# Performance work log

Measured on AMD Instinct MI355X. Metric: run time of the kernel, lower is better.

Reference implementation:

```python
import jax, jax.numpy as jnp
import numpy as np

H = 1024   # hidden size
E = 8      # num experts
B, S = 4, 2048


def setup_inputs() -> dict:
    key = jax.random.key(0)
    k1, k2, k3, k4 = jax.random.split(key, 4)
    x = jax.random.normal(k1, (B, S, H), dtype=jnp.float32)
    wg = jax.random.normal(k2, (H, E), dtype=jnp.float32) * 0.02      # gate weight
    W = jax.random.normal(k3, (E, H, H), dtype=jnp.float32) * 0.02    # expert Linear weights (out, in) per expert
    b = jax.random.normal(k4, (E, H), dtype=jnp.float32) * 0.02       # expert Linear biases
    return {"x": x, "wg": wg, "W": W, "b": b}


def reference(x, wg, W, b):
    Bb, Ss, Hh = x.shape
    Ee = wg.shape[1]
    T = Bb * Ss
    C = T // Ee  # capacity (capacity_factor = 1.0, top-1)

    xt = x.reshape(T, Hh)
    logits = xt @ wg                                   # [T, E]
    probs = jax.nn.softmax(logits, axis=-1)            # [T, E]
    idx = jnp.argmax(probs, axis=-1)                   # [T] top-1 expert
    mask = jax.nn.one_hot(idx, Ee, dtype=xt.dtype)     # [T, E]

    # position of each token within its expert's queue (0-based)
    locations = jnp.cumsum(mask, axis=0) - mask        # [T, E]
    # drop tokens over capacity
    mask = mask * (locations < C).astype(xt.dtype)
    gate = jnp.sum(probs * mask, axis=-1)              # [T] gate prob (0 if dropped)
    loc_s = jnp.sum(locations * mask, axis=-1).astype(jnp.int32)  # [T]
    loc_oh = jax.nn.one_hot(loc_s, C, dtype=xt.dtype)  # [T, C]

    dispatch = mask[:, :, None] * loc_oh[:, None, :]   # [T, E, C]
    combine = gate[:, None, None] * dispatch           # [T, E, C]

    # dispatch tokens -> per-expert buffers [E, C, H]
    exp_in = jnp.einsum('tec,th->ech', dispatch, xt)
    # per-expert Linear: y = x @ W_e^T + b_e
    exp_out = jnp.einsum('ech,efh->ecf', exp_in, W) + b[:, None, :]
    # combine back to tokens, scaled by gate prob
    out = jnp.einsum('tec,ecf->tf', combine, exp_out)  # [T, H]
    return out.reshape(Bb, Ss, Hh)
```

## Files before the change

kernel.cpp:

```cpp
#include <hip/hip_runtime.h>

#define H 1024
#define E 8
#define T 8192
#define CAP 1024

typedef __bf16 bf16x8 __attribute__((ext_vector_type(8)));
typedef float  f32x4  __attribute__((ext_vector_type(4)));
typedef unsigned short u16;

__device__ __forceinline__ u16 f2bf(float f) {
    union { float f; unsigned u; } v; v.f = f;
    unsigned r = v.u + 0x7FFFu + ((v.u >> 16) & 1u);
    return (u16)(r >> 16);
}

typedef __attribute__((address_space(1))) const void* gas_t;
typedef __attribute__((address_space(3))) void* las_t;
__device__ __forceinline__ void gld16(const void* g, void* l) {
    __builtin_amdgcn_global_load_lds((gas_t)g, (las_t)l, 16, 0, 0);
}

#define GATE_BLOCKS 512
#define CVT_BLOCKS  1536

__global__ __launch_bounds__(256) void gatecvt_kernel(
    const float* __restrict__ x, const float* __restrict__ wg,
    const float* __restrict__ W,
    int* __restrict__ eid, float* __restrict__ gate,
    u16* __restrict__ xbf, u16* __restrict__ Wbf) {
    const int tid = threadIdx.x;

    if (blockIdx.x >= GATE_BLOCKS) {
        int i = (blockIdx.x - GATE_BLOCKS) * 256 + tid;
        const int n4 = E * H * H / 4;
        const int stride = CVT_BLOCKS * 256;
        for (; i < n4; i += stride) {
            float4 v = ((const float4*)W)[i];
            ushort4 o;
            o.x = f2bf(v.x); o.y = f2bf(v.y); o.z = f2bf(v.z); o.w = f2bf(v.w);
            ((ushort4*)Wbf)[i] = o;
        }
        return;
    }

    const int wv = tid >> 6, lane = tid & 63;
    const int tbase = blockIdx.x * 16 + wv * 4;
    const int h00 = lane * 4;

    float a[4][8];
    #pragma unroll
    for (int j = 0; j < 4; ++j)
        #pragma unroll
        for (int e = 0; e < 8; ++e) a[j][e] = 0.f;

    #pragma unroll
    for (int q = 0; q < 4; ++q) {
        const int h0 = q * 256 + h00;
        float4 xv[4];
        #pragma unroll
        for (int j = 0; j < 4; ++j)
            xv[j] = *(const float4*)(x + (size_t)(tbase + j) * H + h0);
        #pragma unroll
        for (int j = 0; j < 4; ++j) {
            ushort4 o;
            o.x = f2bf(xv[j].x); o.y = f2bf(xv[j].y);
            o.z = f2bf(xv[j].z); o.w = f2bf(xv[j].w);
            *(ushort4*)(xbf + (size_t)(tbase + j) * H + h0) = o;
        }
        float wr[4][8];
        #pragma unroll
        for (int r = 0; r < 4; ++r) {
            const float4* p = (const float4*)(wg + (size_t)(h0 + r) * E);
            float4 lo = p[0], hi = p[1];
            wr[r][0] = lo.x; wr[r][1] = lo.y; wr[r][2] = lo.z; wr[r][3] = lo.w;
            wr[r][4] = hi.x; wr[r][5] = hi.y; wr[r][6] = hi.z; wr[r][7] = hi.w;
        }
        #pragma unroll
        for (int e = 0; e < 8; ++e)
            #pragma unroll
            for (int j = 0; j < 4; ++j)
                a[j][e] += xv[j].x * wr[0][e] + xv[j].y * wr[1][e]
                         + xv[j].z * wr[2][e] + xv[j].w * wr[3][e];
    }

    const bool b0 = lane & 1, b1 = lane & 2, b2 = lane & 4;
    const int elane = ((lane & 1) << 2) | (lane & 2) | ((lane >> 2) & 1);

    #pragma unroll
    for (int j = 0; j < 4; ++j) {
        float* A = a[j];
        #pragma unroll
        for (int k = 0; k < 4; ++k) {
            float t = b0 ? A[k] : A[k + 4];
            t = __shfl_xor(t, 1);
            A[k] = (b0 ? A[k + 4] : A[k]) + t;
        }
        #pragma unroll
        for (int k = 0; k < 2; ++k) {
            float t = b1 ? A[k] : A[k + 2];
            t = __shfl_xor(t, 2);
            A[k] = (b1 ? A[k + 2] : A[k]) + t;
        }
        {
            float t = b2 ? A[0] : A[1];
            t = __shfl_xor(t, 4);
            A[0] = (b2 ? A[1] : A[0]) + t;
        }
        float v = A[0];
        v += __shfl_xor(v, 8); v += __shfl_xor(v, 16); v += __shfl_xor(v, 32);
        float m = v; int mi = elane;
        #pragma unroll
        for (int off = 1; off <= 4; off <<= 1) {
            float om = __shfl_xor(m, off);
            int   oi = __shfl_xor(mi, off);
            if (om > m || (om == m && oi < mi)) { m = om; mi = oi; }
        }
        float s = expf(v - m);
        s += __shfl_xor(s, 1); s += __shfl_xor(s, 2); s += __shfl_xor(s, 4);
        if (lane == 0) {
            eid[tbase + j]  = mi;
            gate[tbase + j] = 1.0f / s;
        }
    }
}

#define SCAN_T 1024
#define STPT 8
__global__ __launch_bounds__(1024) void scan_kernel(
    const int* __restrict__ eid, float* __restrict__ gate,
    int* __restrict__ perm) {
    __shared__ int cnt[SCAN_T][E];
    __shared__ int part[E][32];
    const int tid = threadIdx.x;

    for (int i = tid; i < E * CAP; i += SCAN_T) perm[i] = -1;

    const int t0 = tid * STPT;
    int ei[STPT];
    #pragma unroll
    for (int i = 0; i < STPT; ++i) ei[i] = eid[t0 + i];

    int c[E];
    #pragma unroll
    for (int e = 0; e < E; ++e) c[e] = 0;
    #pragma unroll
    for (int i = 0; i < STPT; ++i)
        #pragma unroll
        for (int e = 0; e < E; ++e) c[e] += (ei[i] == e);
    #pragma unroll
    for (int e = 0; e < E; ++e) cnt[tid][e] = c[e];
    __syncthreads();

    if (tid < 256) {
        const int e = tid >> 5, g = tid & 31;
        int s = 0;
        for (int i = g * 32; i < g * 32 + 32; ++i) s += cnt[i][e];
        part[e][g] = s;
    }
    __syncthreads();
    if (tid < E) {
        int run = 0;
        #pragma unroll
        for (int g = 0; g < 32; ++g) { int v = part[tid][g]; part[tid][g] = run; run += v; }
    }
    __syncthreads();
    if (tid < 256) {
        const int e = tid >> 5, g = tid & 31;
        int run = part[e][g];
        for (int i = g * 32; i < g * 32 + 32; ++i) { int v = cnt[i][e]; cnt[i][e] = run; run += v; }
    }
    __syncthreads();

    #pragma unroll
    for (int e = 0; e < E; ++e) c[e] = cnt[tid][e];
    #pragma unroll
    for (int i = 0; i < STPT; ++i) {
        const int t = t0 + i, e0 = ei[i];
        int pos = 0;
        #pragma unroll
        for (int k = 0; k < E; ++k) if (e0 == k) pos = c[k]++;
        if (pos < CAP) perm[e0 * CAP + pos] = t;
        else gate[t] = 0.f;
    }
}

__global__ __launch_bounds__(512, 2) void moe_gemm_bf(
    const u16* __restrict__ xbf, const u16* __restrict__ Wbf,
    const float* __restrict__ bias, const int* __restrict__ perm,
    const float* __restrict__ gate, float* __restrict__ out) {
    __shared__ __align__(16) u16 As[3][256 * 64];
    __shared__ __align__(16) u16 Bs[3][128 * 64];
    __shared__ int   perm_s[256];
    __shared__ float gate_s[256];

    const int tid = threadIdx.x;
    const int bid = blockIdx.x;

    if (bid < 64) {
        const int t = bid * 128 + (tid >> 2);
        if (gate[t] == 0.f) {
            const int part = tid & 3;
            float4 z = make_float4(0.f, 0.f, 0.f, 0.f);
            float4* o = (float4*)(out + (size_t)t * H + part * 256);
            #pragma unroll
            for (int i = 0; i < 64; ++i) o[i] = z;
        }
        return;
    }

    const int idx = bid - 64;
    const int e  = idx & 7;
    const int mb = (idx >> 3) & 3;
    const int fb = idx >> 5;

    if (tid < 256) {
        const int t = perm[e * CAP + mb * 256 + tid];
        perm_s[tid] = t;
        gate_s[tid] = (t >= 0) ? gate[t] : 0.f;
    }
    __syncthreads();

    const int lane = tid & 63;
    const int wv = tid >> 6;
    const int wm2 = wv >> 1;
    const int wn2 = wv & 1;
    const int l16 = lane & 15, quad = lane >> 4;

    const int rl  = lane >> 3;
    const int cch = lane & 7;
    const int gch = cch ^ rl;

    const u16* ga[4];
    #pragma unroll
    for (int q = 0; q < 4; ++q) {
        const int r = q * 64 + wv * 8 + rl;
        const int tA = perm_s[r];
        const int tok = tA >= 0 ? tA : 0;
        ga[q] = xbf + (size_t)tok * H + gch * 8;
    }
    const u16* gb[2];
    #pragma unroll
    for (int q = 0; q < 2; ++q) {
        const int r = fb * 128 + q * 64 + wv * 8 + rl;
        gb[q] = Wbf + (size_t)e * H * H + (size_t)r * H + gch * 8;
    }

#define STAGE(BUF, TT)                                                        \
    {                                                                         \
        _Pragma("unroll")                                                     \
        for (int q = 0; q < 4; ++q)                                           \
            gld16(ga[q] + (TT) * 64, &As[BUF][(q * 64 + wv * 8) * 64 + lane * 8]); \
        _Pragma("unroll")                                                     \
        for (int q = 0; q < 2; ++q)                                           \
            gld16(gb[q] + (TT) * 64, &Bs[BUF][(q * 64 + wv * 8) * 64 + lane * 8]); \
    }

    f32x4 acc[4][4] = {};

    STAGE(0, 0)
    STAGE(1, 1)
    asm volatile("s_waitcnt vmcnt(6)" ::: "memory");
    __builtin_amdgcn_sched_barrier(0);
    __builtin_amdgcn_s_barrier();
    __builtin_amdgcn_sched_barrier(0);

    int cur = 0;
    #pragma unroll 1
    for (int t = 0; t < 16; ++t) {
        int nx2 = cur + 2; if (nx2 >= 3) nx2 -= 3;
        if (t < 14) STAGE(nx2, t + 2)

        const u16* cA = As[cur];
        const u16* cB = Bs[cur];
        #pragma unroll
        for (int kh = 0; kh < 2; ++kh) {
            bf16x8 af[4], bf[4];
            const int cc = (kh * 4 + quad) ^ (l16 & 7);
            #pragma unroll
            for (int mi = 0; mi < 4; ++mi)
                af[mi] = *(const bf16x8*)&cA[(wm2 * 64 + mi * 16 + l16) * 64 + cc * 8];
            #pragma unroll
            for (int ni = 0; ni < 4; ++ni)
                bf[ni] = *(const bf16x8*)&cB[(wn2 * 64 + ni * 16 + l16) * 64 + cc * 8];
            #pragma unroll
            for (int mi = 0; mi < 4; ++mi)
                #pragma unroll
                for (int ni = 0; ni < 4; ++ni)
                    acc[mi][ni] = __builtin_amdgcn_mfma_f32_16x16x32_bf16(
                        af[mi], bf[ni], acc[mi][ni], 0, 0, 0);
        }
        if (t == 15) break;

        __builtin_amdgcn_sched_barrier(0);
        if (t < 14) asm volatile("s_waitcnt vmcnt(6)" ::: "memory");
        else        asm volatile("s_waitcnt vmcnt(0)" ::: "memory");
        __builtin_amdgcn_sched_barrier(0);
        __builtin_amdgcn_s_barrier();
        __builtin_amdgcn_sched_barrier(0);
        cur = (cur == 2) ? 0 : cur + 1;
    }
#undef STAGE

    float bv[4];
    #pragma unroll
    for (int ni = 0; ni < 4; ++ni)
        bv[ni] = bias[e * H + fb * 128 + wn2 * 64 + ni * 16 + l16];

    #pragma unroll
    for (int mi = 0; mi < 4; ++mi) {
        #pragma unroll
        for (int r = 0; r < 4; ++r) {
            const int rowl = wm2 * 64 + mi * 16 + quad * 4 + r;
            const int t = perm_s[rowl];
            if (t < 0) continue;
            const float g = gate_s[rowl];
            float* orow = out + (size_t)t * H + fb * 128 + wn2 * 64;
            #pragma unroll
            for (int ni = 0; ni < 4; ++ni)
                orow[ni * 16 + l16] = g * (acc[mi][ni][r] + bv[ni]);
        }
    }
}

extern "C" void kernel_launch(void* const* d_in, const int* in_sizes, int n_in,
                              void* d_out, int out_size, void* d_ws, size_t ws_size,
                              hipStream_t stream) {
    const float* x    = (const float*)d_in[0];
    const float* wg   = (const float*)d_in[1];
    const float* W    = (const float*)d_in[2];
    const float* bias = (const float*)d_in[3];
    float* out = (float*)d_out;

    int*   eid  = (int*)d_ws;
    float* gate = (float*)((char*)d_ws + (size_t)T * 4);
    int*   perm = (int*)((char*)d_ws + (size_t)T * 8);
    u16*   xbf  = (u16*)((char*)d_ws + (size_t)T * 12);
    u16*   Wbf  = xbf + (size_t)T * H;

    gatecvt_kernel<<<GATE_BLOCKS + CVT_BLOCKS, 256, 0, stream>>>(
        x, wg, W, eid, gate, xbf, Wbf);
    scan_kernel<<<1, SCAN_T, 0, stream>>>(eid, gate, perm);
    moe_gemm_bf<<<64 + 256, 512, 0, stream>>>(xbf, Wbf, bias, perm, gate, out);
}
```

Before: 158.9 us.

## Shrink GEMM tiles to 128x128 with double buffering for more blocks and occupancy

The expert GEMM tile drops from 256x128 to 128x128 with two LDS buffers instead of three, so the grid doubles to 512 compute blocks and launch bounds allow 4 blocks per CU. Each wave now computes a 64x32 sub-tile, and MFMA sections get raised wave priority via s_setprio. The aim is better CU fill on 256 CUs and more waves to hide latency. In exchange each tile reuses less data, global traffic for W rises, and the shallower prefetch waits on vmcnt(0) every step.

```diff
diff --git a/kernel.cpp b/kernel.cpp
--- a/kernel.cpp
+++ b/kernel.cpp
@@ -185,14 +185,14 @@
     }
 }
 
-__global__ __launch_bounds__(512, 2) void moe_gemm_bf(
+__global__ __launch_bounds__(512, 4) void moe_gemm_bf(
     const u16* __restrict__ xbf, const u16* __restrict__ Wbf,
     const float* __restrict__ bias, const int* __restrict__ perm,
     const float* __restrict__ gate, float* __restrict__ out) {
-    __shared__ __align__(16) u16 As[3][256 * 64];
-    __shared__ __align__(16) u16 Bs[3][128 * 64];
-    __shared__ int   perm_s[256];
-    __shared__ float gate_s[256];
+    __shared__ __align__(16) u16 As[2][128 * 64];
+    __shared__ __align__(16) u16 Bs[2][128 * 64];
+    __shared__ int   perm_s[128];
+    __shared__ float gate_s[128];
 
     const int tid = threadIdx.x;
     const int bid = blockIdx.x;
@@ -211,11 +211,11 @@
 
     const int idx = bid - 64;
     const int e  = idx & 7;
-    const int mb = (idx >> 3) & 3;
-    const int fb = idx >> 5;
-
-    if (tid < 256) {
-        const int t = perm[e * CAP + mb * 256 + tid];
+    const int mb = (idx >> 3) & 7;
+    const int fb = idx >> 6;
+
+    if (tid < 128) {
+        const int t = perm[e * CAP + mb * 128 + tid];
         perm_s[tid] = t;
         gate_s[tid] = (t >= 0) ? gate[t] : 0.f;
     }
@@ -223,101 +223,96 @@
 
     const int lane = tid & 63;
     const int wv = tid >> 6;
-    const int wm2 = wv >> 1;
-    const int wn2 = wv & 1;
+    const int wm = wv >> 2;
+    const int wn = wv & 3;
     const int l16 = lane & 15, quad = lane >> 4;
 
     const int rl  = lane >> 3;
     const int cch = lane & 7;
     const int gch = cch ^ rl;
-
-    const u16* ga[4];
-    #pragma unroll
-    for (int q = 0; q < 4; ++q) {
-        const int r = q * 64 + wv * 8 + rl;
+    const u16* ga[2];
+    const u16* gb[2];
+    #pragma unroll
+    for (int q = 0; q < 2; ++q) {
+        const int r = wv * 16 + q * 8 + rl;
         const int tA = perm_s[r];
         const int tok = tA >= 0 ? tA : 0;
         ga[q] = xbf + (size_t)tok * H + gch * 8;
-    }
-    const u16* gb[2];
-    #pragma unroll
-    for (int q = 0; q < 2; ++q) {
-        const int r = fb * 128 + q * 64 + wv * 8 + rl;
-        gb[q] = Wbf + (size_t)e * H * H + (size_t)r * H + gch * 8;
-    }
-
-#define STAGE(BUF, TT)                                                        \
+        gb[q] = Wbf + (size_t)e * H * H + (size_t)(fb * 128 + r) * H + gch * 8;
+    }
+
+#define STAGE(BUF)                                                            \
     {                                                                         \
         _Pragma("unroll")                                                     \
-        for (int q = 0; q < 4; ++q)                                           \
-            gld16(ga[q] + (TT) * 64, &As[BUF][(q * 64 + wv * 8) * 64 + lane * 8]); \
+        for (int q = 0; q < 2; ++q) {                                         \
+            gld16(ga[q], &As[BUF][(wv * 16 + q * 8) * 64 + lane * 8]);        \
+            gld16(gb[q], &Bs[BUF][(wv * 16 + q * 8) * 64 + lane * 8]);        \
+        }                                                                     \
         _Pragma("unroll")                                                     \
-        for (int q = 0; q < 2; ++q)                                           \
-            gld16(gb[q] + (TT) * 64, &Bs[BUF][(q * 64 + wv * 8) * 64 + lane * 8]); \
-    }
-
-    f32x4 acc[4][4] = {};
-
-    STAGE(0, 0)
-    STAGE(1, 1)
-    asm volatile("s_waitcnt vmcnt(6)" ::: "memory");
+        for (int q = 0; q < 2; ++q) { ga[q] += 64; gb[q] += 64; }             \
+    }
+
+    f32x4 acc[4][2] = {};
+
+    STAGE(0)
+    asm volatile("s_waitcnt vmcnt(0)" ::: "memory");
     __builtin_amdgcn_sched_barrier(0);
     __builtin_amdgcn_s_barrier();
     __builtin_amdgcn_sched_barrier(0);
 
-    int cur = 0;
+    int p = 0;
     #pragma unroll 1
     for (int t = 0; t < 16; ++t) {
-        int nx2 = cur + 2; if (nx2 >= 3) nx2 -= 3;
-        if (t < 14) STAGE(nx2, t + 2)
-
-        const u16* cA = As[cur];
-        const u16* cB = Bs[cur];
+        if (t < 15) STAGE(p ^ 1)
+
+        const u16* cA = As[p];
+        const u16* cB = Bs[p];
+        __builtin_amdgcn_s_setprio(1);
         #pragma unroll
         for (int kh = 0; kh < 2; ++kh) {
-            bf16x8 af[4], bf[4];
+            bf16x8 af[4], bfr[2];
             const int cc = (kh * 4 + quad) ^ (l16 & 7);
             #pragma unroll
-            for (int mi = 0; mi < 4; ++mi)
-                af[mi] = *(const bf16x8*)&cA[(wm2 * 64 + mi * 16 + l16) * 64 + cc * 8];
-            #pragma unroll
-            for (int ni = 0; ni < 4; ++ni)
-                bf[ni] = *(const bf16x8*)&cB[(wn2 * 64 + ni * 16 + l16) * 64 + cc * 8];
+            for (int i = 0; i < 4; ++i)
+                af[i] = *(const bf16x8*)&cA[(wm * 64 + i * 16 + l16) * 64 + cc * 8];
+            #pragma unroll
+            for (int i = 0; i < 2; ++i)
+                bfr[i] = *(const bf16x8*)&cB[(wn * 32 + i * 16 + l16) * 64 + cc * 8];
             #pragma unroll
             for (int mi = 0; mi < 4; ++mi)
                 #pragma unroll
-                for (int ni = 0; ni < 4; ++ni)
+                for (int ni = 0; ni < 2; ++ni)
                     acc[mi][ni] = __builtin_amdgcn_mfma_f32_16x16x32_bf16(
-                        af[mi], bf[ni], acc[mi][ni], 0, 0, 0);
-        }
+                        af[mi], bfr[ni], acc[mi][ni], 0, 0, 0);
+        }
+        __builtin_amdgcn_s_setprio(0);
         if (t == 15) break;
 
         __builtin_amdgcn_sched_barrier(0);
-        if (t < 14) asm volatile("s_waitcnt vmcnt(6)" ::: "memory");
-        else        asm volatile("s_waitcnt vmcnt(0)" ::: "memory");
+        asm volatile("s_waitcnt vmcnt(0)" ::: "memory");
         __builtin_amdgcn_sched_barrier(0);
         __builtin_amdgcn_s_barrier();
         __builtin_amdgcn_sched_barrier(0);
-        cur = (cur == 2) ? 0 : cur + 1;
+        p ^= 1;
     }
 #undef STAGE
 
-    float bv[4];
-    #pragma unroll
-    for (int ni = 0; ni < 4; ++ni)
-        bv[ni] = bias[e * H + fb * 128 + wn2 * 64 + ni * 16 + l16];
+    float bv[2];
+    #pragma unroll
+    for (int ni = 0; ni < 2; ++ni)
+        bv[ni] = bias[e * H + fb * 128 + wn * 32 + ni * 16 + l16];
 
     #pragma unroll
     for (int mi = 0; mi < 4; ++mi) {
         #pragma unroll
         for (int r = 0; r < 4; ++r) {
-            const int rowl = wm2 * 64 + mi * 16 + quad * 4 + r;
+            const int rowl = wm * 64 + mi * 16 + quad * 4 + r;
             const int t = perm_s[rowl];
             if (t < 0) continue;
             const float g = gate_s[rowl];
-            float* orow = out + (size_t)t * H + fb * 128 + wn2 * 64;
-            #pragma unroll
-            for (int ni = 0; ni < 4; ++ni)
+            float* orow = out + (size_t)t * H + fb * 128 + wn * 32;
+            #pragma unroll
+            for (int ni = 0; ni < 2; ++ni)
                 orow[ni * 16 + l16] = g * (acc[mi][ni][r] + bv[ni]);
         }
     }
@@ -341,5 +336,5 @@
     gatecvt_kernel<<<GATE_BLOCKS + CVT_BLOCKS, 256, 0, stream>>>(
         x, wg, W, eid, gate, xbf, Wbf);
     scan_kernel<<<1, SCAN_T, 0, stream>>>(eid, gate, perm);
-    moe_gemm_bf<<<64 + 256, 512, 0, stream>>>(xbf, Wbf, bias, perm, gate, out);
-}
+    moe_gemm_bf<<<64 + 512, 512, 0, stream>>>(xbf, Wbf, bias, perm, gate, out);
+}
```

New measurement: 156.0 us. About the same (-1.8%).
